# Kernel optimization log

Hardware: AMD Instinct MI355X
Metric: run time of the kernel (lower is better)

Reference implementation:

```python
import jax, jax.numpy as jnp
import numpy as np

D = 2048; H = 16; KV = 4; HD = D // H  # head_dim=128
EPS = 1e-6; THETA = 10000.0


def _rmsnorm(x, w):
    # x: [..., HD]
    var = jnp.mean(x * x, axis=-1, keepdims=True)
    return x * jax.lax.rsqrt(var + EPS) * w


def _rope(x, cos, sin):
    # x: [B, L, nH, HD]; cos/sin: [L, HD//2]; interleaved-pair rotation
    xe = x[..., 0::2]
    xo = x[..., 1::2]
    c = cos[None, :, None, :]
    s = sin[None, :, None, :]
    re = xe * c - xo * s
    ro = xe * s + xo * c
    return jnp.stack([re, ro], axis=-1).reshape(x.shape)


def setup_inputs() -> dict:
    key = jax.random.key(0)
    ks = jax.random.split(key, 8)
    B, L = 2, 2048
    x = jax.random.normal(ks[0], (B, L, D), dtype=jnp.float32)
    wq = jax.random.normal(ks[1], (D, D), dtype=jnp.float32) * 0.02
    wk = jax.random.normal(ks[2], (KV * HD, D), dtype=jnp.float32) * 0.02
    wv = jax.random.normal(ks[3], (KV * HD, D), dtype=jnp.float32) * 0.02
    wo = jax.random.normal(ks[4], (D, D), dtype=jnp.float32) * 0.02
    q_norm_w = jnp.ones((HD,), dtype=jnp.float32)
    k_norm_w = jnp.ones((HD,), dtype=jnp.float32)
    return {"x": x, "wq": wq, "wk": wk, "wv": wv, "wo": wo,
            "q_norm_w": q_norm_w, "k_norm_w": k_norm_w}


def reference(x, wq, wk, wv, wo, q_norm_w, k_norm_w):
    B, L, _ = x.shape
    G = H // KV  # GQA group size (repeat factor)

    q = (x @ wq.T).reshape(B, L, H, HD)
    k = (x @ wk.T).reshape(B, L, KV, HD)
    v = (x @ wv.T).reshape(B, L, KV, HD)

    q = _rmsnorm(q, q_norm_w)
    k = _rmsnorm(k, k_norm_w)

    # RoPE (positions 0..L-1, prompt path)
    inv_freq = 1.0 / (THETA ** (jnp.arange(0, HD, 2, dtype=jnp.float32) / HD))
    ang = jnp.arange(L, dtype=jnp.float32)[:, None] * inv_freq[None, :]  # [L, HD/2]
    cos, sin = jnp.cos(ang), jnp.sin(ang)
    q = _rope(q, cos, sin)
    k = _rope(k, cos, sin)

    # GQA: q head h attends kv head h // G (== repeat_interleave of k,v)
    qg = q.reshape(B, L, KV, G, HD)
    scale = 1.0 / jnp.sqrt(jnp.float32(HD))
    scores = jnp.einsum('bqkgd,bskd->bkgqs', qg, k) * scale  # [B,KV,G,L,L]

    causal = jnp.tril(jnp.ones((L, L), dtype=bool))
    scores = jnp.where(causal, scores, jnp.finfo(scores.dtype).min)
    p = jax.nn.softmax(scores, axis=-1)

    o = jnp.einsum('bkgqs,bskd->bqkgd', p, v).reshape(B, L, D)
    return o @ wo.T
```

## Files before the change

kernel.cpp:

```cpp
#include <hip/hip_runtime.h>
#include <hip/hip_bf16.h>
#include <stdint.h>
#include <stddef.h>

#define D_DIM 2048
#define H_HEADS 16
#define KV_HEADS 4
#define HEAD_DIM 128
#define SEQ_L 2048
#define BATCH 2
#define NTOK 4096
#define NQK 2560
#define NQKV 3072

typedef __attribute__((ext_vector_type(4))) float f32x4;
typedef __attribute__((ext_vector_type(16))) float f32x16;
typedef __attribute__((ext_vector_type(8))) short bf16x8;

__device__ __forceinline__ unsigned short f2bf(float f) {
  __hip_bfloat16 h = __float2bfloat16(f);
  return *reinterpret_cast<unsigned short*>(&h);
}
__device__ __forceinline__ unsigned pack2(float lo, float hi) {
  return (unsigned)f2bf(lo) | ((unsigned)f2bf(hi) << 16);
}
__device__ __forceinline__ float bf2f(unsigned short s) {
  return __uint_as_float(((unsigned int)s) << 16);
}
__device__ __forceinline__ void plane32swap(unsigned& a, unsigned& b) {
  asm volatile("v_permlane32_swap_b32 %0, %1" : "+v"(a), "+v"(b));
}

__device__ __forceinline__ void async_copy16(const void* g, void* l) {
  __builtin_amdgcn_global_load_lds(
      (__attribute__((address_space(1))) void*)(g),
      (__attribute__((address_space(3))) void*)(l),
      16, 0, 0);
}

__device__ __forceinline__ void cast_seg(const float* __restrict__ src,
                                         unsigned short* __restrict__ dst,
                                         int n4, int gid, int stride) {
  for (int i = gid; i < n4; i += stride) {
    float4 v = *reinterpret_cast<const float4*>(src + i * 4);
    uint2 o;
    o.x = pack2(v.x, v.y);
    o.y = pack2(v.z, v.w);
    *reinterpret_cast<uint2*>(dst + i * 4) = o;
  }
}

__global__ __launch_bounds__(256) void fused_cast_kernel(
    const float* __restrict__ s0, const float* __restrict__ s1,
    const float* __restrict__ s2, const float* __restrict__ s3,
    const float* __restrict__ s4,
    unsigned short* __restrict__ d0, unsigned short* __restrict__ d1,
    unsigned short* __restrict__ d2, unsigned short* __restrict__ d3,
    unsigned short* __restrict__ d4) {
  int gid = blockIdx.x * blockDim.x + threadIdx.x;
  int stride = gridDim.x * blockDim.x;
  cast_seg(s0, d0, (NTOK * D_DIM) / 4, gid, stride);
  cast_seg(s1, d1, (D_DIM * D_DIM) / 4, gid, stride);
  cast_seg(s2, d2, (512 * D_DIM) / 4, gid, stride);
  cast_seg(s3, d3, (512 * D_DIM) / 4, gid, stride);
  cast_seg(s4, d4, (D_DIM * D_DIM) / 4, gid, stride);
}

__global__ __launch_bounds__(256) void rope_table_kernel(float* __restrict__ cosT,
                                                         float* __restrict__ sinT) {
  int i = blockIdx.x * blockDim.x + threadIdx.x;
  if (i >= SEQ_L * 64) return;
  int p = i & 63;
  float l = (float)(i >> 6);
  float inv = powf(10000.0f, -(float)p / 64.0f);
  float ang = l * inv;
  cosT[i] = cosf(ang);
  sinT[i] = sinf(ang);
}

__device__ __forceinline__ void store_out(unsigned short* p, float v) { *p = f2bf(v); }
__device__ __forceinline__ void store_out(float* p, float v) { *p = v; }

template <typename OutT, bool VSPLIT>
__global__ __launch_bounds__(256) void gemm_bt_kernel(const unsigned short* __restrict__ A,
                                                      const unsigned short* __restrict__ B,
                                                      OutT* __restrict__ C,
                                                      unsigned short* __restrict__ vt,
                                                      int M, int N, int K) {
  __shared__ unsigned short Alds[128 * 32];
  __shared__ unsigned short Blds[128 * 32];
  const int tid = threadIdx.x;
  const int wave = tid >> 6;
  const int lane = tid & 63;
  const int l15 = lane & 15;
  const int l4 = lane >> 4;

  const int nwg = gridDim.x * gridDim.y;
  const int orig = blockIdx.y * gridDim.x + blockIdx.x;
  const int cpx = nwg >> 3;
  const int swz = (orig & 7) * cpx + (orig >> 3);
  const int m0 = (swz % gridDim.x) * 128;
  const int n0 = (swz / gridDim.x) * 128;

  const int wm = (wave >> 1) * 64;
  const int wn = (wave & 1) * 64;

  f32x4 acc[4][4] = {};

  const int soff0 = wave * 1024 + lane * 16;

  for (int kt = 0; kt < K; kt += 32) {
#pragma unroll
    for (int inst = 0; inst < 2; ++inst) {
      int off = soff0 + inst * 4096;
      int row = off >> 6;
      int colb = off & 63;
      const char* ga = (const char*)(A + (size_t)(m0 + row) * K + kt) + colb;
      async_copy16(ga, (char*)Alds + off);
      const char* gb = (const char*)(B + (size_t)(n0 + row) * K + kt) + colb;
      async_copy16(gb, (char*)Blds + off);
    }
    __syncthreads();
    bf16x8 af[4], bfr[4];
#pragma unroll
    for (int i = 0; i < 4; ++i)
      af[i] = *reinterpret_cast<const bf16x8*>(Alds + (wm + i * 16 + l15) * 32 + l4 * 8);
#pragma unroll
    for (int j = 0; j < 4; ++j)
      bfr[j] = *reinterpret_cast<const bf16x8*>(Blds + (wn + j * 16 + l15) * 32 + l4 * 8);
#pragma unroll
    for (int i = 0; i < 4; ++i)
#pragma unroll
      for (int j = 0; j < 4; ++j)
        acc[i][j] = __builtin_amdgcn_mfma_f32_16x16x32_bf16(af[i], bfr[j], acc[i][j], 0, 0, 0);
    __syncthreads();
  }

  if (VSPLIT && n0 >= NQK) {
#pragma unroll
    for (int i = 0; i < 4; ++i)
#pragma unroll
      for (int j = 0; j < 4; ++j) {
        int vrow = n0 + wn + j * 16 + l15 - NQK;
        int tok0 = m0 + wm + i * 16 + l4 * 4;
        ushort4 pk;
        pk.x = f2bf(acc[i][j][0]);
        pk.y = f2bf(acc[i][j][1]);
        pk.z = f2bf(acc[i][j][2]);
        pk.w = f2bf(acc[i][j][3]);
        *reinterpret_cast<ushort4*>(vt + (size_t)vrow * NTOK + tok0) = pk;
      }
    return;
  }

  const int cstride = VSPLIT ? NQK : N;
#pragma unroll
  for (int i = 0; i < 4; ++i)
#pragma unroll
    for (int j = 0; j < 4; ++j) {
      int col = n0 + wn + j * 16 + l15;
#pragma unroll
      for (int r = 0; r < 4; ++r) {
        int row = m0 + wm + i * 16 + l4 * 4 + r;
        store_out(C + (size_t)row * cstride + col, acc[i][j][r]);
      }
    }
}

__global__ __launch_bounds__(256) void norm_rope_kernel(unsigned short* __restrict__ qk,
                                                        const float* __restrict__ qw,
                                                        const float* __restrict__ kw,
                                                        const float* __restrict__ cosT,
                                                        const float* __restrict__ sinT) {
  int wid = (blockIdx.x * blockDim.x + threadIdx.x) >> 6;
  int lane = threadIdx.x & 63;
  unsigned short* rowp;
  const float* w;
  int m;
  float sc;
  if (wid < NTOK * H_HEADS) {
    m = wid >> 4;
    int hh = wid & 15;
    rowp = qk + (size_t)m * NQK + hh * HEAD_DIM;
    w = qw;
    sc = 0.08838834764831845f;
  } else {
    int r2 = wid - NTOK * H_HEADS;
    m = r2 >> 2;
    int kvh = r2 & 3;
    rowp = qk + (size_t)m * NQK + D_DIM + kvh * HEAD_DIM;
    w = kw;
    sc = 1.0f;
  }
  int l = m & (SEQ_L - 1);
  unsigned int pair = *reinterpret_cast<const unsigned int*>(rowp + lane * 2);
  float e = bf2f((unsigned short)(pair & 0xffffu));
  float o = bf2f((unsigned short)(pair >> 16));
  float ss = e * e + o * o;
#pragma unroll
  for (int off = 1; off < 64; off <<= 1) ss += __shfl_xor(ss, off);
  float rsn = rsqrtf(ss * (1.0f / 128.0f) + 1e-6f) * sc;
  float we = w[lane * 2], wo_ = w[lane * 2 + 1];
  float c = cosT[l * 64 + lane], s = sinT[l * 64 + lane];
  float xe = e * rsn * we, xo = o * rsn * wo_;
  float re = xe * c - xo * s;
  float ro = xe * s + xo * c;
  *reinterpret_cast<unsigned int*>(rowp + lane * 2) = pack2(re, ro);
}

__global__ __launch_bounds__(256, 3) void attn_kernel(const unsigned short* __restrict__ qk,
                                                      const unsigned short* __restrict__ vt,
                                                      unsigned short* __restrict__ obuf,
                                                      unsigned short* __restrict__ p2,
                                                      float* __restrict__ m1G, float* __restrict__ l1G,
                                                      float* __restrict__ m2G, float* __restrict__ l2G) {
  __shared__ unsigned short Kl[64 * 128];
  __shared__ unsigned short Vl[2][128 * 64];
  __shared__ float invl[128];

  const int tid = threadIdx.x;
  const int w = tid >> 6, lane = tid & 63;
  const int l31 = lane & 31, hi = lane >> 5;

  const int jx = blockIdx.x;
  int qt, seg, kv_begin, kv_end;
  bool split;
  if (jx < 16) {
    split = true;
    qt = 15 - (jx >> 1);
    seg = jx & 1;
    int nt = qt + 1;
    kv_begin = seg * nt;
    kv_end = kv_begin + nt;
  } else {
    split = false;
    seg = 0;
    qt = 23 - jx;
    kv_begin = 0;
    kv_end = 2 * qt + 2;
  }
  const int q0 = qt * 128;

  const int bh = blockIdx.y;
  const int b = bh >> 4, h = bh & 15, kvh = h >> 2;

  const unsigned short* Qg = qk + (size_t)(b * SEQ_L + q0 + w * 32 + l31) * NQK + h * HEAD_DIM;
  const unsigned short* Kg = qk + (size_t)(b * SEQ_L) * NQK + D_DIM + kvh * HEAD_DIM;
  const unsigned short* Vg = vt + (size_t)(kvh * HEAD_DIM) * NTOK + b * SEQ_L;

  bf16x8 qf[8];
#pragma unroll
  for (int kk = 0; kk < 8; ++kk)
    qf[kk] = *reinterpret_cast<const bf16x8*>(Qg + kk * 16 + hi * 8);

  f32x16 accO[4] = {};
  float m_run = -1e30f, l_run = 0.0f;

  const int qmin_w = q0 + w * 32;
  const int qmax_w = qmin_w + 31;
  const int qg = qmin_w + l31;

  auto stageK = [&](int kt) {
#pragma unroll
    for (int i = 0; i < 4; ++i) {
      int o = (i * 256 + tid) * 16;
      int row = o >> 8;
      int scb = (o & 255) ^ ((row & 7) << 4);
      const char* src = (const char*)(Kg + (size_t)(kt * 64 + row) * NQK) + scb;
      async_copy16(src, (char*)Kl + o);
    }
  };
  auto stageV = [&](int vb, int kt) {
#pragma unroll
    for (int i = 0; i < 4; ++i) {
      int o = (i * 256 + tid) * 16;
      int d = o >> 7;
      int skb = (o & 127) ^ ((d & 7) << 4);
      const char* src = (const char*)(Vg + (size_t)d * NTOK + kt * 64) + skb;
      async_copy16(src, (char*)(&Vl[vb][0]) + o);
    }
  };

  stageK(kv_begin);
  stageV(0, kv_begin);
  asm volatile("s_waitcnt vmcnt(0)" ::: "memory");
  __syncthreads();

  int vb = 0;
  for (int kt = kv_begin; kt < kv_end; ++kt) {
    const bool active = (kt * 64 <= qmax_w);
    bf16x8 pa[2][2];

    if (active) {
      f32x16 st[2] = {};
      __builtin_amdgcn_s_setprio(1);
#pragma unroll
      for (int stile = 0; stile < 2; ++stile) {
#pragma unroll
        for (int kk = 0; kk < 8; ++kk) {
          int row = stile * 32 + l31;
          int off = (row << 8) + (((kk << 5) + (hi << 4)) ^ ((l31 & 7) << 4));
          bf16x8 kf = *reinterpret_cast<const bf16x8*>((const char*)Kl + off);
          st[stile] = __builtin_amdgcn_mfma_f32_32x32x16_bf16(kf, qf[kk], st[stile], 0, 0, 0);
        }
      }
      __builtin_amdgcn_s_setprio(0);

      const bool need_mask = (kt * 64 + 63 > qmin_w);
      float tmax = -1e30f;
#pragma unroll
      for (int stile = 0; stile < 2; ++stile)
#pragma unroll
        for (int r = 0; r < 16; ++r) {
          float s = st[stile][r];
          if (need_mask) {
            int key = kt * 64 + stile * 32 + (r & 3) + ((r >> 2) << 3) + (hi << 2);
            if (key > qg) s = -1e30f;
          }
          st[stile][r] = s;
          tmax = fmaxf(tmax, s);
        }
      tmax = fmaxf(tmax, __shfl_xor(tmax, 32));

      if (!__all(tmax - m_run <= 8.0f)) {
        float mnew = fmaxf(m_run, tmax);
        float corr = __expf(m_run - mnew);
        m_run = mnew;
        l_run *= corr;
        float corrq[16];
#pragma unroll
        for (int r = 0; r < 16; ++r) {
          int qi = (r & 3) + ((r >> 2) << 3) + (hi << 2);
          corrq[r] = __shfl(corr, qi);
        }
#pragma unroll
        for (int dt = 0; dt < 4; ++dt)
#pragma unroll
          for (int r = 0; r < 16; ++r) accO[dt][r] *= corrq[r];
      }

      float rsum = 0.0f;
#pragma unroll
      for (int stile = 0; stile < 2; ++stile)
#pragma unroll
        for (int r = 0; r < 16; ++r) {
          float pe = __expf(st[stile][r] - m_run);
          st[stile][r] = pe;
          rsum += pe;
        }
      rsum += __shfl_xor(rsum, 32);
      l_run += rsum;

#pragma unroll
      for (int stile = 0; stile < 2; ++stile)
#pragma unroll
        for (int kc = 0; kc < 2; ++kc) {
          int rb = kc * 8;
          unsigned a  = pack2(st[stile][rb + 0], st[stile][rb + 1]);
          unsigned bw = pack2(st[stile][rb + 4], st[stile][rb + 5]);
          unsigned c  = pack2(st[stile][rb + 2], st[stile][rb + 3]);
          unsigned d  = pack2(st[stile][rb + 6], st[stile][rb + 7]);
          plane32swap(a, bw);
          plane32swap(c, d);
          union { bf16x8 v; unsigned u[4]; } uu;
          uu.u[0] = a; uu.u[1] = c; uu.u[2] = bw; uu.u[3] = d;
          pa[stile][kc] = uu.v;
        }
    }

    if (kt + 1 < kv_end) stageV(vb ^ 1, kt + 1);

    __syncthreads();

    if (kt + 1 < kv_end) stageK(kt + 1);

    if (active) {
      __builtin_amdgcn_s_setprio(1);
#pragma unroll
      for (int dt = 0; dt < 4; ++dt) {
        int drow = dt * 32 + l31;
#pragma unroll
        for (int stile = 0; stile < 2; ++stile)
#pragma unroll
          for (int kc = 0; kc < 2; ++kc) {
            int off = (drow << 7) + (((stile << 6) + (kc << 5) + (hi << 4)) ^ ((l31 & 7) << 4));
            bf16x8 vf = *reinterpret_cast<const bf16x8*>((const char*)(&Vl[vb][0]) + off);
            accO[dt] = __builtin_amdgcn_mfma_f32_32x32x16_bf16(pa[stile][kc], vf, accO[dt], 0, 0, 0);
          }
      }
      __builtin_amdgcn_s_setprio(0);
    }

    asm volatile("s_waitcnt vmcnt(0)" ::: "memory");
    __syncthreads();
    vb ^= 1;
  }

  if (!split) {
    if (hi == 0) invl[w * 32 + l31] = 1.0f / l_run;
    __syncthreads();
#pragma unroll
    for (int dt = 0; dt < 4; ++dt)
#pragma unroll
      for (int r = 0; r < 16; ++r) {
        int qrow = (r & 3) + ((r >> 2) << 3) + (hi << 2);
        float val = accO[dt][r] * invl[w * 32 + qrow];
        int tok = b * SEQ_L + q0 + w * 32 + qrow;
        obuf[(size_t)tok * D_DIM + h * HEAD_DIM + dt * 32 + l31] = f2bf(val);
      }
  } else {
    const int rowbase = bh * 1024 + (qt - 8) * 128;
    if (hi == 0) {
      int rr = rowbase + w * 32 + l31;
      if (seg == 0) { m1G[rr] = m_run; l1G[rr] = l_run; }
      else          { m2G[rr] = m_run; l2G[rr] = l_run; }
    }
#pragma unroll
    for (int dt = 0; dt < 4; ++dt)
#pragma unroll
      for (int r = 0; r < 16; ++r) {
        int qrow = (r & 3) + ((r >> 2) << 3) + (hi << 2);
        float val = accO[dt][r];
        if (seg == 0) {
          int tok = b * SEQ_L + q0 + w * 32 + qrow;
          obuf[(size_t)tok * D_DIM + h * HEAD_DIM + dt * 32 + l31] = f2bf(val);
        } else {
          size_t prow = (size_t)(rowbase + w * 32 + qrow);
          p2[prow * HEAD_DIM + dt * 32 + l31] = f2bf(val);
        }
      }
  }
}

__global__ __launch_bounds__(256) void combine_kernel(unsigned short* __restrict__ obuf,
                                                      const unsigned short* __restrict__ p2,
                                                      const float* __restrict__ m1G, const float* __restrict__ l1G,
                                                      const float* __restrict__ m2G, const float* __restrict__ l2G) {
  int gid = blockIdx.x * blockDim.x + threadIdx.x;
  int row = gid >> 4;
  int dc = (gid & 15) * 8;
  int bh = row >> 10;
  int rem = row & 1023;
  int qt = 8 + (rem >> 7);
  int rr = rem & 127;
  int b = bh >> 4, h = bh & 15;
  size_t tok = (size_t)(b * SEQ_L + qt * 128 + rr);

  float m1 = m1G[row], l1 = l1G[row], m2 = m2G[row], l2 = l2G[row];
  float mm = fmaxf(m1, m2);
  float w1 = __expf(m1 - mm), w2 = __expf(m2 - mm);
  float inv = 1.0f / (w1 * l1 + w2 * l2);

  unsigned short* op = obuf + tok * D_DIM + h * HEAD_DIM + dc;
  const unsigned short* pp = p2 + (size_t)row * HEAD_DIM + dc;
  ushort4 a0 = *reinterpret_cast<const ushort4*>(op);
  ushort4 a1 = *reinterpret_cast<const ushort4*>(op + 4);
  ushort4 b0 = *reinterpret_cast<const ushort4*>(pp);
  ushort4 b1 = *reinterpret_cast<const ushort4*>(pp + 4);
  ushort4 o0, o1;
  o0.x = f2bf((w1 * bf2f(a0.x) + w2 * bf2f(b0.x)) * inv);
  o0.y = f2bf((w1 * bf2f(a0.y) + w2 * bf2f(b0.y)) * inv);
  o0.z = f2bf((w1 * bf2f(a0.z) + w2 * bf2f(b0.z)) * inv);
  o0.w = f2bf((w1 * bf2f(a0.w) + w2 * bf2f(b0.w)) * inv);
  o1.x = f2bf((w1 * bf2f(a1.x) + w2 * bf2f(b1.x)) * inv);
  o1.y = f2bf((w1 * bf2f(a1.y) + w2 * bf2f(b1.y)) * inv);
  o1.z = f2bf((w1 * bf2f(a1.z) + w2 * bf2f(b1.z)) * inv);
  o1.w = f2bf((w1 * bf2f(a1.w) + w2 * bf2f(b1.w)) * inv);
  *reinterpret_cast<ushort4*>(op) = o0;
  *reinterpret_cast<ushort4*>(op + 4) = o1;
}

extern "C" void kernel_launch(void* const* d_in, const int* in_sizes, int n_in,
                              void* d_out, int out_size, void* d_ws, size_t ws_size,
                              hipStream_t stream) {
  const float* x   = (const float*)d_in[0];
  const float* wq  = (const float*)d_in[1];
  const float* wk  = (const float*)d_in[2];
  const float* wv  = (const float*)d_in[3];
  const float* wo  = (const float*)d_in[4];
  const float* qnw = (const float*)d_in[5];
  const float* knw = (const float*)d_in[6];
  float* out = (float*)d_out;

  char* ws = (char*)d_ws;
  unsigned short* Xb    = (unsigned short*)(ws);
  unsigned short* Wqkvb = (unsigned short*)(ws + 16777216);
  unsigned short* Wob   = (unsigned short*)(ws + 29360128);
  unsigned short* QKb   = (unsigned short*)(ws + 37748736);
  unsigned short* VTb   = (unsigned short*)(ws + 58720256);
  unsigned short* Obuf  = (unsigned short*)(ws + 62914560);
  float* cosT = (float*)(ws + 79691776);
  float* sinT = (float*)(ws + 80216064);

  unsigned short* P2 = (unsigned short*)(ws);
  float* m1G = (float*)(ws + 8388608);
  float* l1G = (float*)(ws + 8519680);
  float* m2G = (float*)(ws + 8650752);
  float* l2G = (float*)(ws + 8781824);

  fused_cast_kernel<<<1024, 256, 0, stream>>>(
      x, wq, wk, wv, wo,
      Xb, Wqkvb,
      Wqkvb + (size_t)D_DIM * D_DIM,
      Wqkvb + (size_t)NQK * D_DIM,
      Wob);
  rope_table_kernel<<<512, 256, 0, stream>>>(cosT, sinT);

  dim3 g1(NTOK / 128, NQKV / 128);
  gemm_bt_kernel<unsigned short, true><<<g1, 256, 0, stream>>>(
      Xb, Wqkvb, QKb, VTb, NTOK, NQKV, D_DIM);

  norm_rope_kernel<<<(NTOK * (H_HEADS + KV_HEADS)) / 4, 256, 0, stream>>>(QKb, qnw, knw, cosT, sinT);

  attn_kernel<<<dim3(24, BATCH * H_HEADS), 256, 0, stream>>>(
      QKb, VTb, Obuf, P2, m1G, l1G, m2G, l2G);
  combine_kernel<<<2048, 256, 0, stream>>>(Obuf, P2, m1G, l1G, m2G, l2G);

  dim3 g2(NTOK / 128, D_DIM / 128);
  gemm_bt_kernel<float, false><<<g2, 256, 0, stream>>>(Obuf, Wob, out, nullptr, NTOK, D_DIM, D_DIM);
}
```

Measured before the change: 244.1 us.

## Fuse QK RMSNorm and RoPE into the QKV GEMM epilogue

Folds the per-head RMSNorm, softmax scale and interleaved RoPE into the QKV projection GEMM epilogue. Each 128-column tile is exactly one head, so row sums of squares are reduced across lanes and the two N-waves through a small shared buffer. This removes the separate norm_rope kernel launch and its bf16 read-modify-write pass over Q/K, and normalizes from the fp32 accumulator before rounding. In exchange the epilogue gains an extra barrier, shuffles and scattered cos/sin table loads. The cast kernel grid is also doubled.

```diff
diff --git a/kernel.cpp b/kernel.cpp
--- a/kernel.cpp
+++ b/kernel.cpp
@@ -86,9 +86,14 @@
                                                       const unsigned short* __restrict__ B,
                                                       OutT* __restrict__ C,
                                                       unsigned short* __restrict__ vt,
+                                                      const float* __restrict__ qnw,
+                                                      const float* __restrict__ knw,
+                                                      const float* __restrict__ cosT,
+                                                      const float* __restrict__ sinT,
                                                       int M, int N, int K) {
   __shared__ unsigned short Alds[128 * 32];
   __shared__ unsigned short Blds[128 * 32];
+  __shared__ float ssbuf[2][128];
   const int tid = threadIdx.x;
   const int wave = tid >> 6;
   const int lane = tid & 63;
@@ -153,7 +158,57 @@
     return;
   }
 
-  const int cstride = VSPLIT ? NQK : N;
+  if (VSPLIT) {
+    const bool isQ = (n0 < D_DIM);
+    const float* wnorm = isQ ? qnw : knw;
+    const float sc = isQ ? 0.08838834764831845f : 1.0f;
+
+    float ssp[4][4];
+#pragma unroll
+    for (int i = 0; i < 4; ++i)
+#pragma unroll
+      for (int r = 0; r < 4; ++r) {
+        float s = 0.0f;
+#pragma unroll
+        for (int j = 0; j < 4; ++j) s += acc[i][j][r] * acc[i][j][r];
+#pragma unroll
+        for (int mk = 1; mk <= 8; mk <<= 1) s += __shfl_xor(s, mk);
+        ssp[i][r] = s;
+      }
+    if (l15 == 0) {
+#pragma unroll
+      for (int i = 0; i < 4; ++i)
+#pragma unroll
+        for (int r = 0; r < 4; ++r)
+          ssbuf[wave & 1][wm + i * 16 + l4 * 4 + r] = ssp[i][r];
+    }
+    __syncthreads();
+
+#pragma unroll
+    for (int i = 0; i < 4; ++i)
+#pragma unroll
+      for (int r = 0; r < 4; ++r) {
+        int brow = wm + i * 16 + l4 * 4 + r;
+        float tot = ssbuf[0][brow] + ssbuf[1][brow];
+        float rsn = rsqrtf(tot * (1.0f / 128.0f) + 1e-6f) * sc;
+        int row = m0 + brow;
+        int l = row & (SEQ_L - 1);
+#pragma unroll
+        for (int j = 0; j < 4; ++j) {
+          int colh = wn + j * 16 + l15;
+          float v = acc[i][j][r] * rsn * wnorm[colh];
+          float pr = __shfl_xor(v, 1);
+          int p = colh >> 1;
+          float c = cosT[l * 64 + p], s = sinT[l * 64 + p];
+          float outv = (colh & 1) ? (pr * s + v * c)
+                                  : (v * c - pr * s);
+          C[(size_t)row * NQK + n0 + colh] = f2bf(outv);
+        }
+      }
+    return;
+  }
+
+  const int cstride = N;
 #pragma unroll
   for (int i = 0; i < 4; ++i)
 #pragma unroll
@@ -165,47 +220,6 @@
         store_out(C + (size_t)row * cstride + col, acc[i][j][r]);
       }
     }
-}
-
-__global__ __launch_bounds__(256) void norm_rope_kernel(unsigned short* __restrict__ qk,
-                                                        const float* __restrict__ qw,
-                                                        const float* __restrict__ kw,
-                                                        const float* __restrict__ cosT,
-                                                        const float* __restrict__ sinT) {
-  int wid = (blockIdx.x * blockDim.x + threadIdx.x) >> 6;
-  int lane = threadIdx.x & 63;
-  unsigned short* rowp;
-  const float* w;
-  int m;
-  float sc;
-  if (wid < NTOK * H_HEADS) {
-    m = wid >> 4;
-    int hh = wid & 15;
-    rowp = qk + (size_t)m * NQK + hh * HEAD_DIM;
-    w = qw;
-    sc = 0.08838834764831845f;
-  } else {
-    int r2 = wid - NTOK * H_HEADS;
-    m = r2 >> 2;
-    int kvh = r2 & 3;
-    rowp = qk + (size_t)m * NQK + D_DIM + kvh * HEAD_DIM;
-    w = kw;
-    sc = 1.0f;
-  }
-  int l = m & (SEQ_L - 1);
-  unsigned int pair = *reinterpret_cast<const unsigned int*>(rowp + lane * 2);
-  float e = bf2f((unsigned short)(pair & 0xffffu));
-  float o = bf2f((unsigned short)(pair >> 16));
-  float ss = e * e + o * o;
-#pragma unroll
-  for (int off = 1; off < 64; off <<= 1) ss += __shfl_xor(ss, off);
-  float rsn = rsqrtf(ss * (1.0f / 128.0f) + 1e-6f) * sc;
-  float we = w[lane * 2], wo_ = w[lane * 2 + 1];
-  float c = cosT[l * 64 + lane], s = sinT[l * 64 + lane];
-  float xe = e * rsn * we, xo = o * rsn * wo_;
-  float re = xe * c - xo * s;
-  float ro = xe * s + xo * c;
-  *reinterpret_cast<unsigned int*>(rowp + lane * 2) = pack2(re, ro);
 }
 
 __global__ __launch_bounds__(256, 3) void attn_kernel(const unsigned short* __restrict__ qk,
@@ -498,7 +512,7 @@
   float* m2G = (float*)(ws + 8650752);
   float* l2G = (float*)(ws + 8781824);
 
-  fused_cast_kernel<<<1024, 256, 0, stream>>>(
+  fused_cast_kernel<<<2048, 256, 0, stream>>>(
       x, wq, wk, wv, wo,
       Xb, Wqkvb,
       Wqkvb + (size_t)D_DIM * D_DIM,
@@ -508,14 +522,13 @@
 
   dim3 g1(NTOK / 128, NQKV / 128);
   gemm_bt_kernel<unsigned short, true><<<g1, 256, 0, stream>>>(
-      Xb, Wqkvb, QKb, VTb, NTOK, NQKV, D_DIM);
-
-  norm_rope_kernel<<<(NTOK * (H_HEADS + KV_HEADS)) / 4, 256, 0, stream>>>(QKb, qnw, knw, cosT, sinT);
+      Xb, Wqkvb, QKb, VTb, qnw, knw, cosT, sinT, NTOK, NQKV, D_DIM);
 
   attn_kernel<<<dim3(24, BATCH * H_HEADS), 256, 0, stream>>>(
       QKb, VTb, Obuf, P2, m1G, l1G, m2G, l2G);
   combine_kernel<<<2048, 256, 0, stream>>>(Obuf, P2, m1G, l1G, m2G, l2G);
 
   dim3 g2(NTOK / 128, D_DIM / 128);
-  gemm_bt_kernel<float, false><<<g2, 256, 0, stream>>>(Obuf, Wob, out, nullptr, NTOK, D_DIM, D_DIM);
-}
+  gemm_bt_kernel<float, false><<<g2, 256, 0, stream>>>(
+      Obuf, Wob, out, nullptr, nullptr, nullptr, nullptr, nullptr, NTOK, D_DIM, D_DIM);
+}
```

New measurement: 265.8 us. 8.9% more time.
